# Performance work log

Measured on AMD Instinct MI355X. Metric: run time of the kernel, lower is better.

Reference implementation:

```python
import jax, jax.numpy as jnp
import numpy as np

N_QUBITS = 12
N_LAYERS = 4
DIM = 2 ** N_QUBITS  # 4096
BATCH = 128
NUM_CLASSES = 10


def _rot_matrix(phi, theta, omega):
    # PennyLane Rot(phi, theta, omega) = RZ(omega) @ RY(theta) @ RZ(phi)
    c = jnp.cos(theta * 0.5)
    s = jnp.sin(theta * 0.5)
    ep = jnp.exp(-0.5j * (phi + omega))  # e^{-i(phi+omega)/2}
    em = jnp.exp(0.5j * (phi - omega))   # e^{ i(phi-omega)/2}
    row0 = jnp.stack([ep * c, -em * s])
    row1 = jnp.stack([jnp.conj(em) * s, jnp.conj(ep) * c])
    return jnp.stack([row0, row1]).astype(jnp.complex64)  # (2,2)


def _apply_single(psi, u, q):
    # psi: (B, 2^n); wire 0 is the most-significant bit (PennyLane convention)
    b = psi.shape[0]
    s = psi.reshape(b, 2 ** q, 2, -1)
    s = jnp.einsum('ab,kxbz->kxaz', u, s)
    return s.reshape(b, -1)


def _apply_cnot(psi, c, t, n):
    b = psi.shape[0]
    s = psi.reshape((b,) + (2,) * n)
    ac, at = c + 1, t + 1  # +1 for batch axis
    s0 = jax.lax.index_in_dim(s, 0, ac, keepdims=True)
    s1 = jax.lax.index_in_dim(s, 1, ac, keepdims=True)
    s1 = jnp.flip(s1, axis=at)  # X on target where control == 1
    s = jnp.concatenate([s0, s1], axis=ac)
    return s.reshape(b, -1)


def _pauliz_signs(n):
    idx = np.arange(2 ** n)
    bits = (idx[None, :] >> (n - 1 - np.arange(n)[:, None])) & 1  # wire 0 = MSB
    return jnp.asarray(1.0 - 2.0 * bits, dtype=jnp.float32)  # (n, 2^n)


def setup_inputs() -> dict:
    key = jax.random.key(0)
    k = jax.random.split(key, 6)
    inputs = jax.random.normal(k[0], (BATCH, DIM), dtype=jnp.float32)
    W_pre = jax.random.normal(k[1], (DIM, DIM), dtype=jnp.float32) / np.sqrt(DIM)
    b_pre = jax.random.normal(k[2], (DIM,), dtype=jnp.float32) * 0.01
    q_weights = jax.random.uniform(k[3], (N_LAYERS, N_QUBITS, 3), dtype=jnp.float32,
                                   minval=0.0, maxval=2.0 * np.pi)
    W_fc = jax.random.normal(k[4], (NUM_CLASSES, N_QUBITS), dtype=jnp.float32) / np.sqrt(N_QUBITS)
    b_fc = jax.random.normal(k[5], (NUM_CLASSES,), dtype=jnp.float32) * 0.01
    return {"inputs": inputs, "W_pre": W_pre, "b_pre": b_pre,
            "q_weights": q_weights, "W_fc": W_fc, "b_fc": b_fc}


def reference(inputs, W_pre, b_pre, q_weights, W_fc, b_fc):
    n = N_QUBITS
    # pre_pqc Linear + exact GELU (torch default)
    x = inputs @ W_pre.T + b_pre
    x = jax.nn.gelu(x, approximate=False)
    # AmplitudeEmbedding(normalize=True)
    norm = jnp.sqrt(jnp.sum(x * x, axis=1, keepdims=True))
    psi = (x / norm).astype(jnp.complex64)  # (B, 2^n)
    # N_LAYERS repetitions of StronglyEntanglingLayers (each has N_LAYERS layers)
    for _rep in range(N_LAYERS):
        for l in range(N_LAYERS):
            for q in range(n):
                u = _rot_matrix(q_weights[l, q, 0], q_weights[l, q, 1], q_weights[l, q, 2])
                psi = _apply_single(psi, u, q)
            r = l % (n - 1) + 1  # default ranges of StronglyEntanglingLayers
            for q in range(n):
                psi = _apply_cnot(psi, q, (q + r) % n, n)
    probs = psi.real ** 2 + psi.imag ** 2  # (B, 2^n)
    z = probs @ _pauliz_signs(n).T  # (B, n): <Z_i>
    return z @ W_fc.T + b_fc
```

## Files before the change

kernel.cpp:

```cpp
#include <hip/hip_runtime.h>
#include <math.h>

#define DIM 4096
#define NQ 12
#define BATCH 128
#define BN 32
#define BK 64
#define ZSTR (128 * DIM)

typedef __attribute__((ext_vector_type(8))) short bf16x8;
typedef __attribute__((ext_vector_type(4))) float f32x4;
typedef unsigned int uint2v __attribute__((ext_vector_type(2)));

__device__ __forceinline__ unsigned short f2bf(float f) {
    union { float f; unsigned int u; } c; c.f = f;
    unsigned int u = c.u;
    unsigned int r = u + 0x7fffu + ((u >> 16) & 1u);
    return (unsigned short)(r >> 16);
}

__global__ __launch_bounds__(256) void gemm_bf16_kernel(
    const float* __restrict__ A, const float* __restrict__ W,
    float* __restrict__ psum, int splitk)
{
    __shared__ unsigned short As[128][BK + 8];
    __shared__ unsigned short Bs[BN][BK + 8];

    const int t  = threadIdx.x;
    const int bn = blockIdx.x * BN;
    const int z  = blockIdx.y;
    const int krange = DIM / splitk;
    const int kstart = z * krange;
    const int kend = kstart + krange;
    const int w = t >> 6;
    const int l = t & 63;
    const int m0w = w * 32;

    f32x4 acc[2][2] = {};
    float4 pa[8], pb[2];

    auto load_tiles = [&](int k0) {
#pragma unroll
        for (int i = 0; i < 8; ++i) {
            const int fid = t + i * 256;
            pa[i] = *(const float4*)(A + (size_t)(fid >> 4) * DIM + k0 + (fid & 15) * 4);
        }
#pragma unroll
        for (int i = 0; i < 2; ++i) {
            const int fid = t + i * 256;
            pb[i] = *(const float4*)(W + (size_t)(bn + (fid >> 4)) * DIM + k0 + (fid & 15) * 4);
        }
    };

    load_tiles(kstart);
    for (int k0 = kstart; k0 < kend; k0 += BK) {
        __syncthreads();
#pragma unroll
        for (int i = 0; i < 8; ++i) {
            const int fid = t + i * 256;
            const int row = fid >> 4, c4 = (fid & 15) * 4;
            union { unsigned short h[4]; uint2 u; } pk;
            pk.h[0] = f2bf(pa[i].x); pk.h[1] = f2bf(pa[i].y);
            pk.h[2] = f2bf(pa[i].z); pk.h[3] = f2bf(pa[i].w);
            *(uint2*)&As[row][c4] = pk.u;
        }
#pragma unroll
        for (int i = 0; i < 2; ++i) {
            const int fid = t + i * 256;
            const int row = fid >> 4, c4 = (fid & 15) * 4;
            union { unsigned short h[4]; uint2 u; } pk;
            pk.h[0] = f2bf(pb[i].x); pk.h[1] = f2bf(pb[i].y);
            pk.h[2] = f2bf(pb[i].z); pk.h[3] = f2bf(pb[i].w);
            *(uint2*)&Bs[row][c4] = pk.u;
        }
        const int kn = (k0 + BK < kend) ? (k0 + BK) : k0;
        load_tiles(kn);
        __syncthreads();
#pragma unroll
        for (int kk = 0; kk < 2; ++kk) {
            const int kc = kk * 32 + (l >> 4) * 8;
            bf16x8 a0 = *(const bf16x8*)&As[m0w +      (l & 15)][kc];
            bf16x8 a1 = *(const bf16x8*)&As[m0w + 16 + (l & 15)][kc];
            bf16x8 b0 = *(const bf16x8*)&Bs[      (l & 15)][kc];
            bf16x8 b1 = *(const bf16x8*)&Bs[16 + (l & 15)][kc];
            acc[0][0] = __builtin_amdgcn_mfma_f32_16x16x32_bf16(a0, b0, acc[0][0], 0, 0, 0);
            acc[0][1] = __builtin_amdgcn_mfma_f32_16x16x32_bf16(a0, b1, acc[0][1], 0, 0, 0);
            acc[1][0] = __builtin_amdgcn_mfma_f32_16x16x32_bf16(a1, b0, acc[1][0], 0, 0, 0);
            acc[1][1] = __builtin_amdgcn_mfma_f32_16x16x32_bf16(a1, b1, acc[1][1], 0, 0, 0);
        }
    }
#pragma unroll
    for (int mf = 0; mf < 2; ++mf)
#pragma unroll
        for (int nf = 0; nf < 2; ++nf)
#pragma unroll
            for (int r = 0; r < 4; ++r) {
                const int m = m0w + mf * 16 + (l >> 4) * 4 + r;
                const int n = bn + nf * 16 + (l & 15);
                psum[(size_t)z * ZSTR + (size_t)m * DIM + n] = acc[mf][nf][r];
            }
}

template<int CTRL>
__device__ __forceinline__ float fdpp(float v) {
    return __int_as_float(__builtin_amdgcn_update_dpp(
        0, __float_as_int(v), CTRL, 0xF, 0xF, false));
}
__device__ __forceinline__ float pl16_partner(float v) {
#if __has_builtin(__builtin_amdgcn_permlane16_swap)
    uint2v r = __builtin_amdgcn_permlane16_swap(__float_as_uint(v), __float_as_uint(v), false, false);
    return __uint_as_float(r.x ^ r.y ^ __float_as_uint(v));
#else
    float a = v, b = v;
    asm volatile("v_permlane16_swap_b32 %0, %1" : "+v"(a), "+v"(b));
    return __uint_as_float(__float_as_uint(a) ^ __float_as_uint(b) ^ __float_as_uint(v));
#endif
}
__device__ __forceinline__ float pl32_partner(float v) {
#if __has_builtin(__builtin_amdgcn_permlane32_swap)
    uint2v r = __builtin_amdgcn_permlane32_swap(__float_as_uint(v), __float_as_uint(v), false, false);
    return __uint_as_float(r.x ^ r.y ^ __float_as_uint(v));
#else
    float a = v, b = v;
    asm volatile("v_permlane32_swap_b32 %0, %1" : "+v"(a), "+v"(b));
    return __uint_as_float(__float_as_uint(a) ^ __float_as_uint(b) ^ __float_as_uint(v));
#endif
}

#define F0SWZ(x) ((x) ^ (((x) >> 4) & 3) ^ ((((x) >> 10) & 3) << 2))
__device__ __forceinline__ int f1swz(unsigned int pack, int x) {
    int low = 0;
#pragma unroll
    for (int k = 0; k < 8; ++k)
        low ^= (-((x >> (4 + k)) & 1)) & (int)((pack >> (4 * k)) & 15u);
    return x ^ low;
}

__global__ __launch_bounds__(1024, 4) void circuit_kernel(
    const float* __restrict__ psum, int splitk, const float* __restrict__ bias,
    const float* __restrict__ qw, const float* __restrict__ Wfc,
    const float* __restrict__ bfc, float* __restrict__ out)
{
    __shared__ float2 sbuf[2][4096];
    __shared__ float4 gsel[48][2];
    __shared__ float4 grow1[48];
    __shared__ float redw[16];
    __shared__ float zred[16][12];
    __shared__ float zbit[12];

    const int t = threadIdx.x;
    const int b = blockIdx.x;
    const int wv = t >> 6;
    const int l6 = t & 63;
    const int w01 = wv & 3;
    const int w23 = wv >> 2;

    const unsigned int APACK[4] = {0x84000031u, 0x84000013u, 0x84010021u, 0x84008432u};

    if (t < 48) {
        const int base = t * 3;
        const float phi = qw[base + 0], th = qw[base + 1], om = qw[base + 2];
        float c, s, chp, shp, chm, shm;
        sincosf(0.5f * th, &s, &c);
        sincosf(0.5f * (phi + om), &shp, &chp);
        sincosf(0.5f * (phi - om), &shm, &chm);
        const float u00r =  c * chp, u00i = -c * shp;
        const float u01r = -s * chm, u01i = -s * shm;
        const float u10r =  s * chm, u10i = -s * shm;
        const float u11r =  c * chp, u11i =  c * shp;
        gsel[t][0] = make_float4(u00r, u00i, u01r, u01i);
        gsel[t][1] = make_float4(u11r, u11i, u10r, u10i);
        grow1[t]   = make_float4(u10r, u10i, u11r, u11i);
    }

    int ssfb[4], sspjv[4][4], fwb[4];
    const int s0base = (wv << 8) | (l6 << 2);
    const int s1base = ((l6 & 3) << 10) | ((l6 >> 2) << 4) | (w23 << 2) | w01;
#pragma unroll
    for (int ll = 0; ll < 4; ++ll) {
        const int r = ll + 1;
        int u = s0base;
        for (int q = 11; q >= 0; --q) {
            const int bc = 11 - q, bt2 = 11 - ((q + r) % 12);
            u ^= ((u >> bc) & 1) << bt2;
        }
        ssfb[ll] = f1swz(APACK[ll], u);
        fwb[ll]  = f1swz(APACK[ll], s1base);
        sspjv[ll][0] = 0;
#pragma unroll
        for (int j = 1; j < 4; ++j) {
            int v = j;
            for (int q = 11; q >= 0; --q) {
                const int bc = 11 - q, bt2 = 11 - ((q + r) % 12);
                v ^= ((v >> bc) & 1) << bt2;
            }
            sspjv[ll][j] = f1swz(APACK[ll], v);
        }
    }

    const int base0 = F0SWZ(s0base);
    const int base1 = F0SWZ(s1base);

    const int bs0 = l6 & 1, bs1 = (l6 >> 1) & 1, bs2 = (l6 >> 2) & 1;
    const int bs3 = (l6 >> 3) & 1, bs4 = (l6 >> 4) & 1, bs5 = (l6 >> 5) & 1;

    float a0 = 0.f, a1 = 0.f, a2 = 0.f, a3 = 0.f;
    for (int z = 0; z < splitk; ++z) {
        const float4 p = *(const float4*)(psum + (size_t)z * ZSTR + (size_t)b * DIM + t * 4);
        a0 += p.x; a1 += p.y; a2 += p.z; a3 += p.w;
    }
    {
        const float4 bb = *(const float4*)(bias + t * 4);
        a0 += bb.x; a1 += bb.y; a2 += bb.z; a3 += bb.w;
    }
    float xr[4];
    xr[0] = 0.5f * a0 * (1.0f + erff(a0 * 0.70710678118654752f));
    xr[1] = 0.5f * a1 * (1.0f + erff(a1 * 0.70710678118654752f));
    xr[2] = 0.5f * a2 * (1.0f + erff(a2 * 0.70710678118654752f));
    xr[3] = 0.5f * a3 * (1.0f + erff(a3 * 0.70710678118654752f));
    float ss = xr[0]*xr[0] + xr[1]*xr[1] + xr[2]*xr[2] + xr[3]*xr[3];
#pragma unroll
    for (int off = 32; off; off >>= 1) ss += __shfl_xor(ss, off);
    if (l6 == 0) redw[wv] = ss;
    __syncthreads();
    float tot = 0.f;
#pragma unroll
    for (int i = 0; i < 16; ++i) tot += redw[i];
    const float rn = 1.0f / sqrtf(tot);

    float sr[4], si[4];
#pragma unroll
    for (int j = 0; j < 4; ++j) { sr[j] = xr[j] * rn; si[j] = 0.f; }

    auto reg_gate = [&](int lb, float4 g0, float4 g1) {
#pragma unroll
        for (int p = 0; p < 2; ++p) {
            const int j0 = (lb == 0) ? (p << 1) : p;
            const int j1 = j0 | (1 << lb);
            const float ar = sr[j0], ai = si[j0];
            const float br = sr[j1], bi = si[j1];
            sr[j0] = g0.x * ar - g0.y * ai + g0.z * br - g0.w * bi;
            si[j0] = g0.x * ai + g0.y * ar + g0.z * bi + g0.w * br;
            sr[j1] = g1.x * ar - g1.y * ai + g1.z * br - g1.w * bi;
            si[j1] = g1.x * ai + g1.y * ar + g1.z * bi + g1.w * br;
        }
    };
    auto lane_gate = [&](auto&& partner, float4 gs) {
#pragma unroll
        for (int j = 0; j < 4; ++j) {
            const float pr = partner(sr[j]), pi = partner(si[j]);
            const float nr = gs.x * sr[j] - gs.y * si[j] + gs.z * pr - gs.w * pi;
            const float ni = gs.x * si[j] + gs.y * sr[j] + gs.z * pi + gs.w * pr;
            sr[j] = nr; si[j] = ni;
        }
    };

    for (int rep = 0; rep < 4; ++rep) {
#pragma unroll
        for (int l = 0; l < 4; ++l) {
            const int gb = l * 12;
            const float4 gA2 = gsel[gb + 9][bs0], gA3 = gsel[gb + 8][bs1];
            const float4 gA4 = gsel[gb + 7][bs2], gA5 = gsel[gb + 6][bs3];
            const float4 gA6 = gsel[gb + 5][bs4], gA7 = gsel[gb + 4][bs5];
            const float4 rAa0 = gsel[gb + 11][0], rAb0 = grow1[gb + 11];
            const float4 rAa1 = gsel[gb + 10][0], rAb1 = grow1[gb + 10];
            lane_gate([](float v) { return fdpp<0xB1>(v); },               gA2);
            lane_gate([](float v) { return fdpp<0x4E>(v); },               gA3);
            lane_gate([](float v) { return fdpp<0x1B>(fdpp<0x141>(v)); },  gA4);
            lane_gate([](float v) { return fdpp<0x141>(fdpp<0x140>(v)); }, gA5);
            lane_gate([](float v) { return pl16_partner(v); },             gA6);
            lane_gate([](float v) { return pl32_partner(v); },             gA7);
            reg_gate(0, rAa0, rAb0);
            reg_gate(1, rAa1, rAb1);
#pragma unroll
            for (int j = 0; j < 4; ++j)
                sbuf[0][base0 ^ j] = make_float2(sr[j], si[j]);
            __syncthreads();
#pragma unroll
            for (int j = 0; j < 4; ++j) {
                float2 a = sbuf[0][base1 ^ (j << 8)];
                sr[j] = a.x; si[j] = a.y;
            }
            const float4 gB0 = gsel[gb + 1][bs0], gB1 = gsel[gb + 0][bs1];
            const float4 rBa0 = gsel[gb + 3][0], rBb0 = grow1[gb + 3];
            const float4 rBa1 = gsel[gb + 2][0], rBb1 = grow1[gb + 2];
            lane_gate([](float v) { return fdpp<0xB1>(v); }, gB0);
            lane_gate([](float v) { return fdpp<0x4E>(v); }, gB1);
            reg_gate(0, rBa0, rBb0);
            reg_gate(1, rBa1, rBb1);
#pragma unroll
            for (int j = 0; j < 4; ++j)
                sbuf[1][fwb[l] ^ (j << 8) ^ ((l == 2) ? (j & 1) : 0)] = make_float2(sr[j], si[j]);
            __syncthreads();
#pragma unroll
            for (int j = 0; j < 4; ++j) {
                float2 a = sbuf[1][ssfb[l] ^ sspjv[l][j]];
                sr[j] = a.x; si[j] = a.y;
            }
        }
    }

    const float p0 = sr[0]*sr[0] + si[0]*si[0];
    const float p1 = sr[1]*sr[1] + si[1]*si[1];
    const float p2 = sr[2]*sr[2] + si[2]*si[2];
    const float p3 = sr[3]*sr[3] + si[3]*si[3];
    const float psumv = p0 + p1 + p2 + p3;
    float zp[12];
    zp[0] = p0 - p1 + p2 - p3;
    zp[1] = p0 + p1 - p2 - p3;
#pragma unroll
    for (int bp = 2; bp < 12; ++bp)
        zp[bp] = ((t >> (bp - 2)) & 1) ? -psumv : psumv;
#pragma unroll
    for (int bp = 0; bp < 12; ++bp) {
        float vv = zp[bp];
#pragma unroll
        for (int off = 32; off; off >>= 1) vv += __shfl_xor(vv, off);
        if (l6 == 0) zred[wv][bp] = vv;
    }
    __syncthreads();
    if (t < 12) {
        float vv = 0.f;
#pragma unroll
        for (int w2 = 0; w2 < 16; ++w2) vv += zred[w2][t];
        zbit[t] = vv;
    }
    __syncthreads();
    if (t < 10) {
        float o = bfc[t];
#pragma unroll
        for (int q = 0; q < NQ; ++q) o = fmaf(zbit[11 - q], Wfc[t * NQ + q], o);
        out[b * 10 + t] = o;
    }
}

extern "C" void kernel_launch(void* const* d_in, const int* in_sizes, int n_in,
                              void* d_out, int out_size, void* d_ws, size_t ws_size,
                              hipStream_t stream)
{
    const float* inputs = (const float*)d_in[0];
    const float* W_pre  = (const float*)d_in[1];
    const float* b_pre  = (const float*)d_in[2];
    const float* q_w    = (const float*)d_in[3];
    const float* W_fc   = (const float*)d_in[4];
    const float* b_fc   = (const float*)d_in[5];
    float* outp = (float*)d_out;
    float* psum = (float*)d_ws;

    const size_t slab = (size_t)ZSTR * sizeof(float);
    int splitk = 4;
    if (ws_size < 4 * slab) splitk = 2;
    if (ws_size < 2 * slab) splitk = 1;

    dim3 g1(DIM / BN, splitk);
    gemm_bf16_kernel<<<g1, 256, 0, stream>>>(inputs, W_pre, psum, splitk);
    circuit_kernel<<<BATCH, 1024, 0, stream>>>(psum, splitk, b_pre, q_w, W_fc, b_fc, outp);
}
```

Measured before the change: 108.9 us.

## Pack complex gate math into v_pk_fma, use hw bf16 convert, raise split-K

The circuit kernel now holds amplitudes as float2 and applies each 2x2 complex gate with packed-FP32 inline asm (v_pk_mul/v_pk_fma). Gate coefficients are precomputed in a sign-expanded layout so that each output costs four packed ops. The GEMM replaces the manual bf16 rounding with the HIP __float22bfloat162_rn intrinsic. Split-K rises to 8 when the workspace allows it, and the occupancy hint on the circuit kernel's launch bounds is dropped. Together these aim to cut VALU instruction count and add GEMM parallelism, at the cost of more partial-sum traffic and extra LDS reads for the larger gate table.

```diff
diff --git a/kernel.cpp b/kernel.cpp
--- a/kernel.cpp
+++ b/kernel.cpp
@@ -1,4 +1,5 @@
 #include <hip/hip_runtime.h>
+#include <hip/hip_bf16.h>
 #include <math.h>
 
 #define DIM 4096
@@ -12,11 +13,11 @@
 typedef __attribute__((ext_vector_type(4))) float f32x4;
 typedef unsigned int uint2v __attribute__((ext_vector_type(2)));
 
-__device__ __forceinline__ unsigned short f2bf(float f) {
-    union { float f; unsigned int u; } c; c.f = f;
-    unsigned int u = c.u;
-    unsigned int r = u + 0x7fffu + ((u >> 16) & 1u);
-    return (unsigned short)(r >> 16);
+__device__ __forceinline__ uint2 cvt4bf(float4 v) {
+    union { __hip_bfloat162 h2[2]; uint2 u; } pk;
+    pk.h2[0] = __float22bfloat162_rn(make_float2(v.x, v.y));
+    pk.h2[1] = __float22bfloat162_rn(make_float2(v.z, v.w));
+    return pk.u;
 }
 
 __global__ __launch_bounds__(256) void gemm_bf16_kernel(
@@ -58,20 +59,12 @@
 #pragma unroll
         for (int i = 0; i < 8; ++i) {
             const int fid = t + i * 256;
-            const int row = fid >> 4, c4 = (fid & 15) * 4;
-            union { unsigned short h[4]; uint2 u; } pk;
-            pk.h[0] = f2bf(pa[i].x); pk.h[1] = f2bf(pa[i].y);
-            pk.h[2] = f2bf(pa[i].z); pk.h[3] = f2bf(pa[i].w);
-            *(uint2*)&As[row][c4] = pk.u;
+            *(uint2*)&As[fid >> 4][(fid & 15) * 4] = cvt4bf(pa[i]);
         }
 #pragma unroll
         for (int i = 0; i < 2; ++i) {
             const int fid = t + i * 256;
-            const int row = fid >> 4, c4 = (fid & 15) * 4;
-            union { unsigned short h[4]; uint2 u; } pk;
-            pk.h[0] = f2bf(pb[i].x); pk.h[1] = f2bf(pb[i].y);
-            pk.h[2] = f2bf(pb[i].z); pk.h[3] = f2bf(pb[i].w);
-            *(uint2*)&Bs[row][c4] = pk.u;
+            *(uint2*)&Bs[fid >> 4][(fid & 15) * 4] = cvt4bf(pb[i]);
         }
         const int kn = (k0 + BK < kend) ? (k0 + BK) : k0;
         load_tiles(kn);
@@ -127,6 +120,21 @@
 #endif
 }
 
+__device__ __forceinline__ float2 pk_cplx(float4 e1, float4 e2, float2 A, float2 B) {
+    float2 t;
+    float2 e1xy = make_float2(e1.x, e1.y), e1zw = make_float2(e1.z, e1.w);
+    float2 e2xy = make_float2(e2.x, e2.y), e2zw = make_float2(e2.z, e2.w);
+    asm("v_pk_mul_f32 %0, %1, %2 op_sel:[0,0] op_sel_hi:[0,1]"
+        : "=v"(t) : "v"(e1xy), "v"(A));
+    asm("v_pk_fma_f32 %0, %1, %2, %0 op_sel:[0,1,0] op_sel_hi:[1,0,1]"
+        : "+v"(t) : "v"(e2xy), "v"(A));
+    asm("v_pk_fma_f32 %0, %1, %2, %0 op_sel:[0,0,0] op_sel_hi:[0,1,1]"
+        : "+v"(t) : "v"(e1zw), "v"(B));
+    asm("v_pk_fma_f32 %0, %1, %2, %0 op_sel:[0,1,0] op_sel_hi:[1,0,1]"
+        : "+v"(t) : "v"(e2zw), "v"(B));
+    return t;
+}
+
 #define F0SWZ(x) ((x) ^ (((x) >> 4) & 3) ^ ((((x) >> 10) & 3) << 2))
 __device__ __forceinline__ int f1swz(unsigned int pack, int x) {
     int low = 0;
@@ -136,14 +144,13 @@
     return x ^ low;
 }
 
-__global__ __launch_bounds__(1024, 4) void circuit_kernel(
+__global__ __launch_bounds__(1024) void circuit_kernel(
     const float* __restrict__ psum, int splitk, const float* __restrict__ bias,
     const float* __restrict__ qw, const float* __restrict__ Wfc,
     const float* __restrict__ bfc, float* __restrict__ out)
 {
     __shared__ float2 sbuf[2][4096];
-    __shared__ float4 gsel[48][2];
-    __shared__ float4 grow1[48];
+    __shared__ float4 ge[48][2][2];
     __shared__ float redw[16];
     __shared__ float zred[16][12];
     __shared__ float zbit[12];
@@ -168,9 +175,10 @@
         const float u01r = -s * chm, u01i = -s * shm;
         const float u10r =  s * chm, u10i = -s * shm;
         const float u11r =  c * chp, u11i =  c * shp;
-        gsel[t][0] = make_float4(u00r, u00i, u01r, u01i);
-        gsel[t][1] = make_float4(u11r, u11i, u10r, u10i);
-        grow1[t]   = make_float4(u10r, u10i, u11r, u11i);
+        ge[t][0][0] = make_float4(u00r, 0.f, u01r, 0.f);
+        ge[t][0][1] = make_float4(-u00i, u00i, -u01i, u01i);
+        ge[t][1][0] = make_float4(u11r, 0.f, u10r, 0.f);
+        ge[t][1][1] = make_float4(-u11i, u11i, -u10i, u10i);
     }
 
     int ssfb[4], sspjv[4][4], fwb[4];
@@ -228,30 +236,25 @@
     for (int i = 0; i < 16; ++i) tot += redw[i];
     const float rn = 1.0f / sqrtf(tot);
 
-    float sr[4], si[4];
-#pragma unroll
-    for (int j = 0; j < 4; ++j) { sr[j] = xr[j] * rn; si[j] = 0.f; }
-
-    auto reg_gate = [&](int lb, float4 g0, float4 g1) {
+    float2 S[4];
+#pragma unroll
+    for (int j = 0; j < 4; ++j) S[j] = make_float2(xr[j] * rn, 0.f);
+
+    auto lane_gate = [&](auto&& partner, float4 e1, float4 e2) {
+#pragma unroll
+        for (int j = 0; j < 4; ++j) {
+            float2 P = make_float2(partner(S[j].x), partner(S[j].y));
+            S[j] = pk_cplx(e1, e2, S[j], P);
+        }
+    };
+    auto reg_gate = [&](int lb, float4 e10, float4 e20, float4 e11, float4 e21) {
 #pragma unroll
         for (int p = 0; p < 2; ++p) {
             const int j0 = (lb == 0) ? (p << 1) : p;
             const int j1 = j0 | (1 << lb);
-            const float ar = sr[j0], ai = si[j0];
-            const float br = sr[j1], bi = si[j1];
-            sr[j0] = g0.x * ar - g0.y * ai + g0.z * br - g0.w * bi;
-            si[j0] = g0.x * ai + g0.y * ar + g0.z * bi + g0.w * br;
-            sr[j1] = g1.x * ar - g1.y * ai + g1.z * br - g1.w * bi;
-            si[j1] = g1.x * ai + g1.y * ar + g1.z * bi + g1.w * br;
-        }
-    };
-    auto lane_gate = [&](auto&& partner, float4 gs) {
-#pragma unroll
-        for (int j = 0; j < 4; ++j) {
-            const float pr = partner(sr[j]), pi = partner(si[j]);
-            const float nr = gs.x * sr[j] - gs.y * si[j] + gs.z * pr - gs.w * pi;
-            const float ni = gs.x * si[j] + gs.y * sr[j] + gs.z * pi + gs.w * pr;
-            sr[j] = nr; si[j] = ni;
+            const float2 A = S[j0], B = S[j1];
+            S[j0] = pk_cplx(e10, e20, A, B);
+            S[j1] = pk_cplx(e11, e21, B, A);
         }
     };
 
@@ -259,51 +262,39 @@
 #pragma unroll
         for (int l = 0; l < 4; ++l) {
             const int gb = l * 12;
-            const float4 gA2 = gsel[gb + 9][bs0], gA3 = gsel[gb + 8][bs1];
-            const float4 gA4 = gsel[gb + 7][bs2], gA5 = gsel[gb + 6][bs3];
-            const float4 gA6 = gsel[gb + 5][bs4], gA7 = gsel[gb + 4][bs5];
-            const float4 rAa0 = gsel[gb + 11][0], rAb0 = grow1[gb + 11];
-            const float4 rAa1 = gsel[gb + 10][0], rAb1 = grow1[gb + 10];
-            lane_gate([](float v) { return fdpp<0xB1>(v); },               gA2);
-            lane_gate([](float v) { return fdpp<0x4E>(v); },               gA3);
-            lane_gate([](float v) { return fdpp<0x1B>(fdpp<0x141>(v)); },  gA4);
-            lane_gate([](float v) { return fdpp<0x141>(fdpp<0x140>(v)); }, gA5);
-            lane_gate([](float v) { return pl16_partner(v); },             gA6);
-            lane_gate([](float v) { return pl32_partner(v); },             gA7);
-            reg_gate(0, rAa0, rAb0);
-            reg_gate(1, rAa1, rAb1);
+            lane_gate([](float v) { return fdpp<0xB1>(v); },               ge[gb + 9][bs0][0], ge[gb + 9][bs0][1]);
+            lane_gate([](float v) { return fdpp<0x4E>(v); },               ge[gb + 8][bs1][0], ge[gb + 8][bs1][1]);
+            lane_gate([](float v) { return fdpp<0x1B>(fdpp<0x141>(v)); },  ge[gb + 7][bs2][0], ge[gb + 7][bs2][1]);
+            lane_gate([](float v) { return fdpp<0x141>(fdpp<0x140>(v)); }, ge[gb + 6][bs3][0], ge[gb + 6][bs3][1]);
+            lane_gate([](float v) { return pl16_partner(v); },             ge[gb + 5][bs4][0], ge[gb + 5][bs4][1]);
+            lane_gate([](float v) { return pl32_partner(v); },             ge[gb + 4][bs5][0], ge[gb + 4][bs5][1]);
+            reg_gate(0, ge[gb + 11][0][0], ge[gb + 11][0][1], ge[gb + 11][1][0], ge[gb + 11][1][1]);
+            reg_gate(1, ge[gb + 10][0][0], ge[gb + 10][0][1], ge[gb + 10][1][0], ge[gb + 10][1][1]);
 #pragma unroll
             for (int j = 0; j < 4; ++j)
-                sbuf[0][base0 ^ j] = make_float2(sr[j], si[j]);
+                sbuf[0][base0 ^ j] = S[j];
             __syncthreads();
 #pragma unroll
-            for (int j = 0; j < 4; ++j) {
-                float2 a = sbuf[0][base1 ^ (j << 8)];
-                sr[j] = a.x; si[j] = a.y;
-            }
-            const float4 gB0 = gsel[gb + 1][bs0], gB1 = gsel[gb + 0][bs1];
-            const float4 rBa0 = gsel[gb + 3][0], rBb0 = grow1[gb + 3];
-            const float4 rBa1 = gsel[gb + 2][0], rBb1 = grow1[gb + 2];
-            lane_gate([](float v) { return fdpp<0xB1>(v); }, gB0);
-            lane_gate([](float v) { return fdpp<0x4E>(v); }, gB1);
-            reg_gate(0, rBa0, rBb0);
-            reg_gate(1, rBa1, rBb1);
-#pragma unroll
             for (int j = 0; j < 4; ++j)
-                sbuf[1][fwb[l] ^ (j << 8) ^ ((l == 2) ? (j & 1) : 0)] = make_float2(sr[j], si[j]);
+                S[j] = sbuf[0][base1 ^ (j << 8)];
+            lane_gate([](float v) { return fdpp<0xB1>(v); }, ge[gb + 1][bs0][0], ge[gb + 1][bs0][1]);
+            lane_gate([](float v) { return fdpp<0x4E>(v); }, ge[gb + 0][bs1][0], ge[gb + 0][bs1][1]);
+            reg_gate(0, ge[gb + 3][0][0], ge[gb + 3][0][1], ge[gb + 3][1][0], ge[gb + 3][1][1]);
+            reg_gate(1, ge[gb + 2][0][0], ge[gb + 2][0][1], ge[gb + 2][1][0], ge[gb + 2][1][1]);
+#pragma unroll
+            for (int j = 0; j < 4; ++j)
+                sbuf[1][fwb[l] ^ (j << 8) ^ ((l == 2) ? (j & 1) : 0)] = S[j];
             __syncthreads();
 #pragma unroll
-            for (int j = 0; j < 4; ++j) {
-                float2 a = sbuf[1][ssfb[l] ^ sspjv[l][j]];
-                sr[j] = a.x; si[j] = a.y;
-            }
-        }
-    }
-
-    const float p0 = sr[0]*sr[0] + si[0]*si[0];
-    const float p1 = sr[1]*sr[1] + si[1]*si[1];
-    const float p2 = sr[2]*sr[2] + si[2]*si[2];
-    const float p3 = sr[3]*sr[3] + si[3]*si[3];
+            for (int j = 0; j < 4; ++j)
+                S[j] = sbuf[1][ssfb[l] ^ sspjv[l][j]];
+        }
+    }
+
+    const float p0 = S[0].x*S[0].x + S[0].y*S[0].y;
+    const float p1 = S[1].x*S[1].x + S[1].y*S[1].y;
+    const float p2 = S[2].x*S[2].x + S[2].y*S[2].y;
+    const float p3 = S[3].x*S[3].x + S[3].y*S[3].y;
     const float psumv = p0 + p1 + p2 + p3;
     float zp[12];
     zp[0] = p0 - p1 + p2 - p3;
@@ -348,7 +339,8 @@
     float* psum = (float*)d_ws;
 
     const size_t slab = (size_t)ZSTR * sizeof(float);
-    int splitk = 4;
+    int splitk = 8;
+    if (ws_size < 8 * slab) splitk = 4;
     if (ws_size < 4 * slab) splitk = 2;
     if (ws_size < 2 * slab) splitk = 1;
 
```

Result: faster. 104.8 us (-3.7%).
